# Kernel optimization log

Measured on AMD Instinct MI355X. Metric: run time of the kernel, lower is better.

Reference implementation:

```python
import jax, jax.numpy as jnp
import numpy as np

B, S, DIM, H, D = 4, 2048, 1024, 16, 64
WINDOW = 512  # max_mem_segments * window_size


def _rotary_angles(seq_len, dim_head):
    inv_freq = 1.0 / (10000.0 ** (jnp.arange(0, dim_head, 2, dtype=jnp.float32) / dim_head))
    freqs = jnp.arange(seq_len, dtype=jnp.float32)[:, None] * inv_freq[None, :]  # [S, D/2]
    return jnp.repeat(freqs, 2, axis=-1)  # [S, D] interleaved


def _rotate_half(x):
    x1 = x[..., 0::2]
    x2 = x[..., 1::2]
    return jnp.stack((-x2, x1), axis=-1).reshape(x.shape)


def _apply_rotary(x, angles):
    # x: [b h n d], angles: [n d]
    return x * jnp.cos(angles) + _rotate_half(x) * jnp.sin(angles)


def setup_inputs() -> dict:
    key = jax.random.key(0)
    ks = jax.random.split(key, 7)
    tokens = jax.random.normal(ks[0], (B, S, DIM), dtype=jnp.float32)
    value_residual = jax.random.normal(ks[1], (B, H, S, D), dtype=jnp.float32)
    s = 0.02
    Wq = jax.random.normal(ks[2], (DIM, H * D), dtype=jnp.float32) * s
    Wkv = jax.random.normal(ks[3], (DIM, 2 * H * D), dtype=jnp.float32) * s
    Wout = jax.random.normal(ks[4], (H * D, DIM), dtype=jnp.float32) * s
    Wgate = jax.random.normal(ks[5], (DIM, H), dtype=jnp.float32) * s
    Wmix = jax.random.normal(ks[6], (DIM, H), dtype=jnp.float32) * s
    return {"tokens": tokens, "value_residual": value_residual, "Wq": Wq,
            "Wkv": Wkv, "Wout": Wout, "Wgate": Wgate, "Wmix": Wmix}


def reference(tokens, value_residual, Wq, Wkv, Wout, Wgate, Wmix):
    b, n, dim = tokens.shape
    scale = D ** -0.5

    def split_heads(t):  # [b n (h d)] -> [b h n d]
        return t.reshape(b, n, H, D).transpose(0, 2, 1, 3)

    q = split_heads(tokens @ Wq)
    kv = tokens @ Wkv
    k = split_heads(kv[..., : H * D])
    v = split_heads(kv[..., H * D:])

    q = q * scale

    # value-residual lerp: v.lerp(value_residual, mix)
    mix = jax.nn.sigmoid(jnp.einsum('bnd,dh->bhn', tokens, Wmix))[..., None]  # [b h n 1]
    v = v + (value_residual - v) * mix

    angles = _rotary_angles(n, D)
    q = _apply_rotary(q, angles)
    k = _apply_rotary(k, angles)

    sim = jnp.einsum('bhid,bhjd->bhij', q, k)

    # fixed-window causal mask: dist = i - j; masked if dist < 0 or dist > WINDOW
    pos = jnp.arange(n)
    dist = pos[:, None] - pos[None, :]
    mask = (dist < 0) | (dist > WINDOW)
    neg = -jnp.finfo(sim.dtype).max
    sim = jnp.where(mask[None, None], neg, sim)

    attn = jax.nn.softmax(sim, axis=-1)
    out = jnp.einsum('bhij,bhjd->bhid', attn, v)

    gates = jax.nn.sigmoid(jnp.einsum('bnd,dh->bhn', tokens, Wgate))[..., None]  # [b h n 1]
    out = out * gates

    out = out.transpose(0, 2, 1, 3).reshape(b, n, H * D)
    return out @ Wout
```

## Files before the change

kernel.cpp:

```cpp
#include <hip/hip_runtime.h>

#define NH 16
#define SLEN 2048
#define DMODEL 1024
#define DHEAD 64
#define WIN 512
#define NB 4

typedef unsigned short u16;
typedef unsigned int u32;
typedef unsigned long long u64;
typedef __attribute__((ext_vector_type(8))) __bf16 bf16x8;
typedef __attribute__((ext_vector_type(4))) float floatx4;

__device__ __forceinline__ float b2f(u32 bits16) {
  union { u32 i; float f; } x; x.i = bits16 << 16; return x.f;
}
__device__ __forceinline__ u16 f2b(float f) {
  union { float f; u32 i; } x; x.f = f;
  u32 r = x.i + 0x7fffu + ((x.i >> 16) & 1u);
  return (u16)(r >> 16);
}

__device__ __forceinline__ void gl2lds16(const u16* g, u16* l) {
  __builtin_amdgcn_global_load_lds(
      (const __attribute__((address_space(1))) unsigned int*)g,
      (__attribute__((address_space(3))) unsigned int*)l, 16, 0, 0);
}

template<int OFF>
__device__ __forceinline__ bf16x8 ldsr128(u32 addr) {
  bf16x8 r;
  if constexpr (OFF == 0)
    asm volatile("ds_read_b128 %0, %1" : "=v"(r) : "v"(addr));
  else
    asm volatile("ds_read_b128 %0, %1 offset:%2" : "=v"(r) : "v"(addr), "i"(OFF));
  return r;
}

#define WAIT_VM6   asm volatile("s_waitcnt vmcnt(6)" ::: "memory")
#define WAIT_VM0   asm volatile("s_waitcnt vmcnt(0)" ::: "memory")
#define WAIT_LGKM8 asm volatile("s_waitcnt lgkmcnt(8)" ::: "memory")
#define WAIT_LGKM0 asm volatile("s_waitcnt lgkmcnt(0)" ::: "memory")
#define SCHEDB     __builtin_amdgcn_sched_barrier(0)

__global__ __launch_bounds__(256) void prep_all(
    const float* __restrict__ tokens, const float* __restrict__ Wq,
    const float* __restrict__ Wkv, const float* __restrict__ Wout,
    const float* __restrict__ Wmix, const float* __restrict__ Wgate,
    u64* __restrict__ tokA64, u16* __restrict__ WqkvT, u16* __restrict__ WoutT,
    u16* __restrict__ Wmg, float2* __restrict__ rtab) {
  __shared__ u16 T[64][72];
  const int blk = blockIdx.x, tid = threadIdx.x;
  if (blk < 8192) {
    int i = blk * 256 + tid;
    float4 f = reinterpret_cast<const float4*>(tokens)[i];
    union { u16 u[4]; u64 ll; } pk;
    pk.u[0] = f2b(f.x); pk.u[1] = f2b(f.y); pk.u[2] = f2b(f.z); pk.u[3] = f2b(f.w);
    tokA64[i] = pk.ll;
  } else if (blk < 9216) {
    const float* src; u16* dst; int ld, nb, n0, k0;
    if (blk < 8960) {
      int tile = blk - 8192;
      n0 = (tile % 48) * 64; k0 = (tile / 48) * 64;
      if (n0 < 1024) { src = Wq; ld = 1024; nb = n0; }
      else { src = Wkv; ld = 2048; nb = n0 - 1024; }
      dst = WqkvT;
    } else {
      int tile = blk - 8960;
      n0 = (tile % 16) * 64; k0 = (tile / 16) * 64;
      src = Wout; ld = 1024; nb = n0; dst = WoutT;
    }
#pragma unroll
    for (int i = 0; i < 16; ++i) {
      int e = i * 256 + tid;
      int kr = e >> 6, nc = e & 63;
      T[kr][nc] = f2b(src[(size_t)(k0 + kr) * ld + nb + nc]);
    }
    __syncthreads();
#pragma unroll
    for (int i = 0; i < 16; ++i) {
      int e = i * 256 + tid;
      int nr = e >> 6, kc = e & 63;
      dst[(size_t)(n0 + nr) * 1024 + k0 + kc] = T[kc][nr];
    }
  } else if (blk < 9344) {
    int idx = (blk - 9216) * 256 + tid;
    int n = idx >> 10, k = idx & 1023;
    float v = (n < 16) ? Wmix[k * 16 + n] : Wgate[k * 16 + (n - 16)];
    Wmg[idx] = f2b(v);
  } else {
    int idx = (blk - 9344) * 256 + tid;
    int s = idx >> 5, t = idx & 31;
    float inv = __expf((float)t * -0.2878231366f);
    float ang = (float)s * inv;
    float sn, cs;
    __sincosf(ang, &sn, &cs);
    rtab[idx] = make_float2(cs, sn);
  }
}

__global__ __launch_bounds__(128) void mixgate_mfma(const u16* __restrict__ A,
    const u16* __restrict__ Wmg, float* __restrict__ mixws, float* __restrict__ gatews) {
  const int lane = threadIdx.x & 63, w = threadIdx.x >> 6;
  const int lm = lane & 15, quad = lane >> 4;
  const int row0 = (blockIdx.x * 2 + w) * 16;

  floatx4 acc[2];
  acc[0] = (floatx4){0.f, 0.f, 0.f, 0.f};
  acc[1] = (floatx4){0.f, 0.f, 0.f, 0.f};

#pragma unroll 4
  for (int k0 = 0; k0 < 1024; k0 += 32) {
    bf16x8 af = *reinterpret_cast<const bf16x8*>(
        &A[(size_t)(row0 + lm) * 1024 + k0 + quad * 8]);
    bf16x8 bf[2];
#pragma unroll
    for (int nt = 0; nt < 2; ++nt)
      bf[nt] = *reinterpret_cast<const bf16x8*>(
          &Wmg[(size_t)(nt * 16 + lm) * 1024 + k0 + quad * 8]);
#pragma unroll
    for (int nt = 0; nt < 2; ++nt)
      acc[nt] = __builtin_amdgcn_mfma_f32_16x16x32_bf16(af, bf[nt], acc[nt], 0, 0, 0);
  }

#pragma unroll
  for (int r = 0; r < 4; ++r) {
    int grow = row0 + quad * 4 + r;
    int b = grow >> 11, s = grow & 2047;
#pragma unroll
    for (int nt = 0; nt < 2; ++nt) {
      int n = nt * 16 + lm;
      float sig = 1.0f / (1.0f + __expf(-acc[nt][r]));
      int h = n & 15;
      (n < 16 ? mixws : gatews)[(b * NH + h) * SLEN + s] = sig;
    }
  }
}

template<int MODE>
__global__ __launch_bounds__(512, 2) void gemm_pipe(
    const u16* __restrict__ A, const u16* __restrict__ Bt,
    float* __restrict__ C,
    u16* __restrict__ qws, u16* __restrict__ kws, u16* __restrict__ vws,
    const float* __restrict__ vres, const float* __restrict__ mixws,
    const float2* __restrict__ rtab, int N) {
  __shared__ u16 smem[73728];
  const int tid = threadIdx.x;
  const int nbx = N >> 7;
  const int wg = (blockIdx.x & 7) * (gridDim.x >> 3) + (blockIdx.x >> 3);
  const int bx = wg % nbx, by = wg / nbx;
  const int row0 = by * 256, col0 = bx * 128;
  const int w = tid >> 6, lane = tid & 63;
  const int wr = (w >> 1) * 64, wc = (w & 1) * 64;
  const int lm = lane & 15, quad = lane >> 4;
  const int NT = 16;
  const int sr = tid >> 3, sc = tid & 7;
  const int sl0 = (sr * 8 + sc) * 8;
  const u16* gA = A + (size_t)(row0 + sr) * 1024 + ((sc ^ (sr & 7)) << 3);
  const u16* gB = Bt + (size_t)(col0 + sr) * 1024 + ((sc ^ (sr & 7)) << 3);

  const u32 ldsbase = (u32)(size_t)(__attribute__((address_space(3))) u16*)smem;
  u32 arow[2], brow[2];
#pragma unroll
  for (int j = 0; j < 2; ++j) {
    u32 cslot = (u32)((j * 4 + quad) ^ (lm & 7));
    arow[j] = (u32)(wr + lm) * 128 + cslot * 16;
    brow[j] = (u32)(wc + lm) * 128 + cslot * 16;
  }

  floatx4 acc[4][4];
#pragma unroll
  for (int i = 0; i < 4; ++i)
#pragma unroll
    for (int j = 0; j < 4; ++j)
      acc[i][j] = (floatx4){0.f, 0.f, 0.f, 0.f};

  auto stage3 = [&](u16* Sa, u16* Sb, int ks, int half) {
    if (half == 0) {
      gl2lds16(gA + ks, Sa + sl0);
      gl2lds16(gA + 65536 + ks, Sa + 4096 + sl0);
      gl2lds16(gB + ks, Sb + sl0);
    } else {
      gl2lds16(gA + 131072 + ks, Sa + 8192 + sl0);
      gl2lds16(gA + 196608 + ks, Sa + 12288 + sl0);
      gl2lds16(gB + 65536 + ks, Sb + 4096 + sl0);
    }
  };

#pragma unroll
  for (int tt = 0; tt < 2; ++tt) {
    u16* Sa = smem + tt * 24576;
    u16* Sb = Sa + 16384;
    stage3(Sa, Sb, tt * 64, 0);
    stage3(Sa, Sb, tt * 64, 1);
  }

  int cur = 0;
  for (int t = 0; t < NT; ++t) {
    int sidx = cur + 2; if (sidx >= 3) sidx -= 3;
    u16* Sa = smem + sidx * 24576;
    u16* Sb = Sa + 16384;
    const int ks = (t + 2) << 6;
    const bool do_stage = t < NT - 2;
    const u32 abase = ldsbase + (u32)cur * 49152u;

    if (t < NT - 1) { WAIT_VM6; } else { WAIT_VM0; }
    __builtin_amdgcn_s_barrier();

    const u32 a0 = abase + arow[0], b0 = abase + 32768u + brow[0];
    const u32 a1 = abase + arow[1], b1 = abase + 32768u + brow[1];
    bf16x8 af0[4], bf0[4], af1[4], bf1[4];
    af0[0] = ldsr128<0>(a0);    af0[1] = ldsr128<2048>(a0);
    af0[2] = ldsr128<4096>(a0); af0[3] = ldsr128<6144>(a0);
    bf0[0] = ldsr128<0>(b0);    bf0[1] = ldsr128<2048>(b0);
    bf0[2] = ldsr128<4096>(b0); bf0[3] = ldsr128<6144>(b0);
    af1[0] = ldsr128<0>(a1);    af1[1] = ldsr128<2048>(a1);
    af1[2] = ldsr128<4096>(a1); af1[3] = ldsr128<6144>(a1);
    bf1[0] = ldsr128<0>(b1);    bf1[1] = ldsr128<2048>(b1);
    bf1[2] = ldsr128<4096>(b1); bf1[3] = ldsr128<6144>(b1);
    if (do_stage) { stage3(Sa, Sb, ks, 0); stage3(Sa, Sb, ks, 1); }
    SCHEDB;
    WAIT_LGKM8;
    SCHEDB;
    __builtin_amdgcn_s_setprio(1);
#pragma unroll
    for (int mt = 0; mt < 4; ++mt)
#pragma unroll
      for (int nt = 0; nt < 4; ++nt)
        acc[mt][nt] = __builtin_amdgcn_mfma_f32_16x16x32_bf16(
            af0[mt], bf0[nt], acc[mt][nt], 0, 0, 0);
    __builtin_amdgcn_s_setprio(0);
    WAIT_LGKM0;
    SCHEDB;
    __builtin_amdgcn_s_setprio(1);
#pragma unroll
    for (int mt = 0; mt < 4; ++mt)
#pragma unroll
      for (int nt = 0; nt < 4; ++nt)
        acc[mt][nt] = __builtin_amdgcn_mfma_f32_16x16x32_bf16(
            af1[mt], bf1[nt], acc[mt][nt], 0, 0, 0);
    __builtin_amdgcn_s_setprio(0);

    cur += 1; if (cur >= 3) cur -= 3;
  }

  if (MODE == 0) {
#pragma unroll
    for (int mt = 0; mt < 4; ++mt)
#pragma unroll
      for (int r = 0; r < 4; ++r) {
        int grow = row0 + wr + mt * 16 + quad * 4 + r;
#pragma unroll
        for (int nt = 0; nt < 4; ++nt)
          C[(size_t)grow * N + col0 + wc + nt * 16 + lm] = acc[mt][nt][r];
      }
  } else {
    const int seg = col0 >> 10;
    if (seg < 2) {
      u16* dst = seg ? kws : qws;
      const float qs = seg ? 1.0f : 0.125f;
      const int colb = (col0 & 1023) + wc;
#pragma unroll
      for (int mt = 0; mt < 4; ++mt)
#pragma unroll
        for (int r = 0; r < 4; ++r) {
          int sg = row0 + wr + mt * 16 + quad * 4 + r;
          int b = sg >> 11, s = sg & 2047;
#pragma unroll
          for (int nt = 0; nt < 4; ++nt) {
            int nn = colb + nt * 16 + lm;
            int h = nn >> 6, d = nn & 63;
            float val = acc[mt][nt][r] * qs;
            float2 cs = rtab[(s << 5) + (d >> 1)];
            float partner = __shfl_xor(val, 1);
            float o = (d & 1) ? fmaf(val, cs.x, partner * cs.y)
                              : fmaf(val, cs.x, -partner * cs.y);
            dst[((size_t)((b * NH + h) * SLEN + s)) * 64 + d] = f2b(o);
          }
        }
    } else {
      const int h0 = (col0 - 2048) >> 6;
      const int p = (w & 1);
      const int b = row0 >> 11, s0 = row0 & 2047;
      const int bh = b * NH + h0 + p;
      u16 (*Vt)[264] = reinterpret_cast<u16(*)[264]>(smem + p * 16896);
      __syncthreads();
#pragma unroll
      for (int mt = 0; mt < 4; ++mt)
#pragma unroll
        for (int nt = 0; nt < 4; ++nt) {
          const int d = nt * 16 + lm;
          const int sl = wr + mt * 16 + quad * 4;
          union { u16 u[4]; u64 ll; } pk;
#pragma unroll
          for (int r = 0; r < 4; ++r) {
            int s = s0 + sl + r;
            float val = acc[mt][nt][r];
            float mv = mixws[bh * SLEN + s];
            float o = val + (vres[((size_t)(bh * SLEN + s)) * 64 + d] - val) * mv;
            pk.u[r] = f2b(o);
          }
          *reinterpret_cast<u64*>(&Vt[d][sl]) = pk.ll;
        }
      __syncthreads();
#pragma unroll
      for (int it = 0; it < 8; ++it) {
        int idx = it * 512 + tid;
        int ph = idx >> 11, rem = idx & 2047;
        int d = rem >> 5, ch = rem & 31;
        const u16* src = smem + ph * 16896 + d * 264 + ch * 8;
        u16* dst = vws + ((size_t)((b * NH + h0 + ph) * 64 + d)) * SLEN + s0 + ch * 8;
        *reinterpret_cast<uint4*>(dst) = *reinterpret_cast<const uint4*>(src);
      }
    }
  }
}

__global__ __launch_bounds__(256) void attn_mfma_kernel(
    const u16* __restrict__ q, const u16* __restrict__ k, const u16* __restrict__ vt,
    const float* __restrict__ gate, u16* __restrict__ X) {
  __shared__ __align__(16) u16 Ks[2][4096];
  __shared__ __align__(16) u16 Vs[2][4096];
  __shared__ __align__(16) u16 Ps[4][16][72];
  const int tid = threadIdx.x;
  const int w = tid >> 6, lane = tid & 63;
  const int lm = lane & 15, quad = lane >> 4;
  const int sid = blockIdx.x;
  const int qt = (sid >> 3) & 31;
  const int bh = ((sid >> 8) << 3) | (sid & 7);
  const int h = bh & 15;
  const int b = bh >> 4;
  const int q0 = qt * 64;
  const size_t kqbase = (size_t)bh * SLEN * 64;
  const size_t vbase  = (size_t)bh * 64 * SLEN;

  bf16x8 qf[2];
  {
    const u16* qrow = q + kqbase + (size_t)(q0 + w * 16 + lm) * 64;
    qf[0] = *reinterpret_cast<const bf16x8*>(qrow + quad * 8);
    qf[1] = *reinterpret_cast<const bf16x8*>(qrow + 32 + quad * 8);
  }

  floatx4 o[4];
#pragma unroll
  for (int nt = 0; nt < 4; ++nt) o[nt] = (floatx4){0.f, 0.f, 0.f, 0.f};
  float lsum = 0.f;
  const int iq = q0 + w * 16 + lm;

  const int c_first = (q0 >= WIN) ? ((q0 - WIN) >> 6) : 0;
  const int c_last = q0 >> 6;

  const int sr = tid >> 3;
  const int scz = ((tid & 7) ^ (sr & 7)) * 8;
  const u32 ksbase = (u32)(size_t)(__attribute__((address_space(3))) u16*)&Ks[0][0];
  const u32 vsbase = (u32)(size_t)(__attribute__((address_space(3))) u16*)&Vs[0][0];
  const u32 psbase = (u32)(size_t)(__attribute__((address_space(3))) u16*)&Ps[0][0][0];
  const int rxa8 = lm & 7;
  const u32 rowoff = (u32)lm * 128 + (u32)((quad ^ rxa8) * 16);
  const u32 paddr = psbase + (u32)(w * 16 + lm) * 144 + (u32)quad * 16;

  auto stage = [&](int c, int buf) {
    const u16* kg = k + kqbase + (size_t)(c << 6) * 64;
    const u16* vg = vt + vbase + (c << 6);
    u16* Kd = &Ks[buf][0]; u16* Vd = &Vs[buf][0];
    gl2lds16(kg + sr * 64 + scz, Kd + tid * 8);
    gl2lds16(kg + (sr + 32) * 64 + scz, Kd + 2048 + tid * 8);
    gl2lds16(vg + (size_t)sr * SLEN + scz, Vd + tid * 8);
    gl2lds16(vg + (size_t)(sr + 32) * SLEN + scz, Vd + 2048 + tid * 8);
  };

  stage(c_first, 0);
  int cur = 0;
  for (int c = c_first; c <= c_last; ++c) {
    const int c0 = c << 6;
    __syncthreads();
    if (c < c_last) stage(c + 1, cur ^ 1);

    const u32 kof = ksbase + (u32)(cur << 13) + rowoff;
    const u32 kof4 = kof ^ 64u;
    bf16x8 k00 = ldsr128<0>(kof),     k01 = ldsr128<2048>(kof),
           k02 = ldsr128<4096>(kof),  k03 = ldsr128<6144>(kof);
    bf16x8 k10 = ldsr128<0>(kof4),    k11 = ldsr128<2048>(kof4),
           k12 = ldsr128<4096>(kof4), k13 = ldsr128<6144>(kof4);
    SCHEDB;
    WAIT_LGKM0;
    SCHEDB;
    floatx4 st[4];
    const floatx4 z4 = (floatx4){0.f, 0.f, 0.f, 0.f};
    __builtin_amdgcn_s_setprio(1);
    st[0] = __builtin_amdgcn_mfma_f32_16x16x32_bf16(k00, qf[0], z4, 0, 0, 0);
    st[0] = __builtin_amdgcn_mfma_f32_16x16x32_bf16(k10, qf[1], st[0], 0, 0, 0);
    st[1] = __builtin_amdgcn_mfma_f32_16x16x32_bf16(k01, qf[0], z4, 0, 0, 0);
    st[1] = __builtin_amdgcn_mfma_f32_16x16x32_bf16(k11, qf[1], st[1], 0, 0, 0);
    st[2] = __builtin_amdgcn_mfma_f32_16x16x32_bf16(k02, qf[0], z4, 0, 0, 0);
    st[2] = __builtin_amdgcn_mfma_f32_16x16x32_bf16(k12, qf[1], st[2], 0, 0, 0);
    st[3] = __builtin_amdgcn_mfma_f32_16x16x32_bf16(k03, qf[0], z4, 0, 0, 0);
    st[3] = __builtin_amdgcn_mfma_f32_16x16x32_bf16(k13, qf[1], st[3], 0, 0, 0);
    __builtin_amdgcn_s_setprio(0);

    const bool need_mask = (c == c_first && q0 >= WIN) || (c == c_last);
    if (need_mask) {
#pragma unroll
      for (int mt = 0; mt < 4; ++mt)
#pragma unroll
        for (int r = 0; r < 4; ++r) {
          int j = c0 + mt * 16 + quad * 4 + r;
          bool valid = (j <= iq) && (j >= iq - WIN);
          if (!valid) st[mt][r] = -3.0e38f;
        }
    }
    float p[4][4], psum = 0.f;
#pragma unroll
    for (int mt = 0; mt < 4; ++mt)
#pragma unroll
      for (int r = 0; r < 4; ++r) {
        p[mt][r] = __expf(st[mt][r]);
        psum += p[mt][r];
      }
    psum += __shfl_xor(psum, 16);
    psum += __shfl_xor(psum, 32);
    lsum += psum;
#pragma unroll
    for (int mt = 0; mt < 4; ++mt) {
      union { u16 u[4]; u64 ll; } pk;
#pragma unroll
      for (int r = 0; r < 4; ++r) pk.u[r] = f2b(p[mt][r]);
      *reinterpret_cast<u64*>(&Ps[w][lm][mt * 16 + quad * 4]) = pk.ll;
    }
    __builtin_amdgcn_wave_barrier();
    __builtin_amdgcn_s_waitcnt(0xC07F);
    __builtin_amdgcn_wave_barrier();

    bf16x8 pa0 = ldsr128<0>(paddr), pa1 = ldsr128<64>(paddr);
    const u32 vof = vsbase + (u32)(cur << 13) + rowoff;
    const u32 vof4 = vof ^ 64u;
    bf16x8 v00 = ldsr128<0>(vof),     v01 = ldsr128<2048>(vof),
           v02 = ldsr128<4096>(vof),  v03 = ldsr128<6144>(vof);
    bf16x8 v10 = ldsr128<0>(vof4),    v11 = ldsr128<2048>(vof4),
           v12 = ldsr128<4096>(vof4), v13 = ldsr128<6144>(vof4);
    SCHEDB;
    WAIT_LGKM0;
    SCHEDB;
    __builtin_amdgcn_s_setprio(1);
    o[0] = __builtin_amdgcn_mfma_f32_16x16x32_bf16(pa0, v00, o[0], 0, 0, 0);
    o[0] = __builtin_amdgcn_mfma_f32_16x16x32_bf16(pa1, v10, o[0], 0, 0, 0);
    o[1] = __builtin_amdgcn_mfma_f32_16x16x32_bf16(pa0, v01, o[1], 0, 0, 0);
    o[1] = __builtin_amdgcn_mfma_f32_16x16x32_bf16(pa1, v11, o[1], 0, 0, 0);
    o[2] = __builtin_amdgcn_mfma_f32_16x16x32_bf16(pa0, v02, o[2], 0, 0, 0);
    o[2] = __builtin_amdgcn_mfma_f32_16x16x32_bf16(pa1, v12, o[2], 0, 0, 0);
    o[3] = __builtin_amdgcn_mfma_f32_16x16x32_bf16(pa0, v03, o[3], 0, 0, 0);
    o[3] = __builtin_amdgcn_mfma_f32_16x16x32_bf16(pa1, v13, o[3], 0, 0, 0);
    __builtin_amdgcn_s_setprio(0);

    cur ^= 1;
  }
  float linv[4], g[4];
#pragma unroll
  for (int r = 0; r < 4; ++r) {
    linv[r] = 1.0f / __shfl(lsum, quad * 4 + r);
    g[r] = gate[bh * SLEN + q0 + w * 16 + quad * 4 + r];
  }
#pragma unroll
  for (int r = 0; r < 4; ++r) {
    int i = q0 + w * 16 + quad * 4 + r;
    u16* xrow = X + ((size_t)(b * SLEN + i)) * 1024 + h * 64;
#pragma unroll
    for (int nt = 0; nt < 4; ++nt)
      xrow[nt * 16 + lm] = f2b(o[nt][r] * linv[r] * g[r]);
  }
}

extern "C" void kernel_launch(void* const* d_in, const int* in_sizes, int n_in,
                              void* d_out, int out_size, void* d_ws, size_t ws_size,
                              hipStream_t stream) {
  (void)in_sizes; (void)n_in; (void)out_size; (void)ws_size;
  const float* tokens = (const float*)d_in[0];
  const float* vres   = (const float*)d_in[1];
  const float* Wq     = (const float*)d_in[2];
  const float* Wkv    = (const float*)d_in[3];
  const float* Wout   = (const float*)d_in[4];
  const float* Wgate  = (const float*)d_in[5];
  const float* Wmix   = (const float*)d_in[6];
  float* out = (float*)d_out;

  char* p = (char*)d_ws;
  auto alloc = [&](size_t bytes) { char* r = p; p += (bytes + 255) & ~(size_t)255; return r; };
  u16*  tokA   = (u16*)alloc(8192ull * 1024 * 2);
  u16*  WqkvT  = (u16*)alloc(3072ull * 1024 * 2);
  u16*  WoutT  = (u16*)alloc(1024ull * 1024 * 2);
  u16*  Wmg    = (u16*)alloc(32ull * 1024 * 2);
  float2* rtab = (float2*)alloc(65536ull * 8);
  u16*  qws    = (u16*)alloc(8388608ull * 2);
  u16*  kws    = (u16*)alloc(8388608ull * 2);
  u16*  vws    = (u16*)alloc(8388608ull * 2);
  u16*  Xws    = (u16*)alloc(8388608ull * 2);
  float* mixws = (float*)alloc(131072ull * 4);
  float* gatews= (float*)alloc(131072ull * 4);

  prep_all<<<9600, 256, 0, stream>>>(tokens, Wq, Wkv, Wout, Wmix, Wgate,
      (u64*)tokA, WqkvT, WoutT, Wmg, rtab);
  mixgate_mfma<<<256, 128, 0, stream>>>(tokA, Wmg, mixws, gatews);
  gemm_pipe<1><<<768, 512, 0, stream>>>(tokA, WqkvT, nullptr,
      qws, kws, vws, vres, mixws, rtab, 3072);
  attn_mfma_kernel<<<2048, 256, 0, stream>>>(qws, kws, vws, gatews, Xws);
  gemm_pipe<0><<<256, 512, 0, stream>>>(Xws, WoutT, out,
      nullptr, nullptr, nullptr, nullptr, nullptr, nullptr, 1024);
}
```

Before: 265.9 us.

## Shrink GEMM tiles to 128x128 with 256 threads and double-buffered LDS

Both projection GEMMs move from a 256x128 tile with 512 threads and a 3-stage LDS ring to a 128x128 tile with 256 threads and two LDS buffers. The next tile is prefetched right after a barrier rather than after issuing LDS reads, and the V-transpose epilogue is resized to match. This doubles the grid (1536 and 512 blocks) for better CU fill and lower LDS use per block. In exchange, each block reuses fewer operands and the pipeline is shallower, with an extra barrier per k-step.

After: 255.0 us. 4.1% less time.

```diff
diff --git a/kernel.cpp b/kernel.cpp
--- a/kernel.cpp
+++ b/kernel.cpp
@@ -38,7 +38,7 @@
   return r;
 }
 
-#define WAIT_VM6   asm volatile("s_waitcnt vmcnt(6)" ::: "memory")
+#define WAIT_VM8   asm volatile("s_waitcnt vmcnt(8)" ::: "memory")
 #define WAIT_VM0   asm volatile("s_waitcnt vmcnt(0)" ::: "memory")
 #define WAIT_LGKM8 asm volatile("s_waitcnt lgkmcnt(8)" ::: "memory")
 #define WAIT_LGKM0 asm volatile("s_waitcnt lgkmcnt(0)" ::: "memory")
@@ -139,18 +139,18 @@
 }
 
 template<int MODE>
-__global__ __launch_bounds__(512, 2) void gemm_pipe(
+__global__ __launch_bounds__(256, 2) void gemm_pipe(
     const u16* __restrict__ A, const u16* __restrict__ Bt,
     float* __restrict__ C,
     u16* __restrict__ qws, u16* __restrict__ kws, u16* __restrict__ vws,
     const float* __restrict__ vres, const float* __restrict__ mixws,
     const float2* __restrict__ rtab, int N) {
-  __shared__ u16 smem[73728];
+  __shared__ u16 smem[32768];
   const int tid = threadIdx.x;
   const int nbx = N >> 7;
   const int wg = (blockIdx.x & 7) * (gridDim.x >> 3) + (blockIdx.x >> 3);
   const int bx = wg % nbx, by = wg / nbx;
-  const int row0 = by * 256, col0 = bx * 128;
+  const int row0 = by * 128, col0 = bx * 128;
   const int w = tid >> 6, lane = tid & 63;
   const int wr = (w >> 1) * 64, wc = (w & 1) * 64;
   const int lm = lane & 15, quad = lane >> 4;
@@ -166,7 +166,7 @@
   for (int j = 0; j < 2; ++j) {
     u32 cslot = (u32)((j * 4 + quad) ^ (lm & 7));
     arow[j] = (u32)(wr + lm) * 128 + cslot * 16;
-    brow[j] = (u32)(wc + lm) * 128 + cslot * 16;
+    brow[j] = 16384u + (u32)(wc + lm) * 128 + cslot * 16;
   }
 
   floatx4 acc[4][4];
@@ -176,40 +176,33 @@
     for (int j = 0; j < 4; ++j)
       acc[i][j] = (floatx4){0.f, 0.f, 0.f, 0.f};
 
-  auto stage3 = [&](u16* Sa, u16* Sb, int ks, int half) {
-    if (half == 0) {
-      gl2lds16(gA + ks, Sa + sl0);
-      gl2lds16(gA + 65536 + ks, Sa + 4096 + sl0);
-      gl2lds16(gB + ks, Sb + sl0);
-    } else {
-      gl2lds16(gA + 131072 + ks, Sa + 8192 + sl0);
-      gl2lds16(gA + 196608 + ks, Sa + 12288 + sl0);
-      gl2lds16(gB + 65536 + ks, Sb + 4096 + sl0);
-    }
+  auto stage8 = [&](int buf, int t2) {
+    const int ks = t2 << 6;
+    u16* Sa = smem + buf * 16384;
+    u16* Sb = Sa + 8192;
+    gl2lds16(gA + ks, Sa + sl0);
+    gl2lds16(gA + 32 * 1024 + ks, Sa + 2048 + sl0);
+    gl2lds16(gA + 64 * 1024 + ks, Sa + 4096 + sl0);
+    gl2lds16(gA + 96 * 1024 + ks, Sa + 6144 + sl0);
+    gl2lds16(gB + ks, Sb + sl0);
+    gl2lds16(gB + 32 * 1024 + ks, Sb + 2048 + sl0);
+    gl2lds16(gB + 64 * 1024 + ks, Sb + 4096 + sl0);
+    gl2lds16(gB + 96 * 1024 + ks, Sb + 6144 + sl0);
   };
 
-#pragma unroll
-  for (int tt = 0; tt < 2; ++tt) {
-    u16* Sa = smem + tt * 24576;
-    u16* Sb = Sa + 16384;
-    stage3(Sa, Sb, tt * 64, 0);
-    stage3(Sa, Sb, tt * 64, 1);
-  }
-
-  int cur = 0;
+  stage8(0, 0);
   for (int t = 0; t < NT; ++t) {
-    int sidx = cur + 2; if (sidx >= 3) sidx -= 3;
-    u16* Sa = smem + sidx * 24576;
-    u16* Sb = Sa + 16384;
-    const int ks = (t + 2) << 6;
-    const bool do_stage = t < NT - 2;
-    const u32 abase = ldsbase + (u32)cur * 49152u;
-
-    if (t < NT - 1) { WAIT_VM6; } else { WAIT_VM0; }
+    const int cur = t & 1;
+    const u32 abase = ldsbase + (u32)cur * 32768u;
+
     __builtin_amdgcn_s_barrier();
-
-    const u32 a0 = abase + arow[0], b0 = abase + 32768u + brow[0];
-    const u32 a1 = abase + arow[1], b1 = abase + 32768u + brow[1];
+    if (t + 1 < NT) { stage8(cur ^ 1, t + 1); WAIT_VM8; }
+    else            { WAIT_VM0; }
+    __builtin_amdgcn_s_barrier();
+    SCHEDB;
+
+    const u32 a0 = abase + arow[0], b0 = abase + brow[0];
+    const u32 a1 = abase + arow[1], b1 = abase + brow[1];
     bf16x8 af0[4], bf0[4], af1[4], bf1[4];
     af0[0] = ldsr128<0>(a0);    af0[1] = ldsr128<2048>(a0);
     af0[2] = ldsr128<4096>(a0); af0[3] = ldsr128<6144>(a0);
@@ -219,7 +212,6 @@
     af1[2] = ldsr128<4096>(a1); af1[3] = ldsr128<6144>(a1);
     bf1[0] = ldsr128<0>(b1);    bf1[1] = ldsr128<2048>(b1);
     bf1[2] = ldsr128<4096>(b1); bf1[3] = ldsr128<6144>(b1);
-    if (do_stage) { stage3(Sa, Sb, ks, 0); stage3(Sa, Sb, ks, 1); }
     SCHEDB;
     WAIT_LGKM8;
     SCHEDB;
@@ -241,8 +233,6 @@
         acc[mt][nt] = __builtin_amdgcn_mfma_f32_16x16x32_bf16(
             af1[mt], bf1[nt], acc[mt][nt], 0, 0, 0);
     __builtin_amdgcn_s_setprio(0);
-
-    cur += 1; if (cur >= 3) cur -= 3;
   }
 
   if (MODE == 0) {
@@ -281,10 +271,10 @@
         }
     } else {
       const int h0 = (col0 - 2048) >> 6;
-      const int p = (w & 1);
+      const int p = w & 1;
       const int b = row0 >> 11, s0 = row0 & 2047;
       const int bh = b * NH + h0 + p;
-      u16 (*Vt)[264] = reinterpret_cast<u16(*)[264]>(smem + p * 16896);
+      u16* VtW = smem + p * 8704;
       __syncthreads();
 #pragma unroll
       for (int mt = 0; mt < 4; ++mt)
@@ -301,17 +291,17 @@
             float o = val + (vres[((size_t)(bh * SLEN + s)) * 64 + d] - val) * mv;
             pk.u[r] = f2b(o);
           }
-          *reinterpret_cast<u64*>(&Vt[d][sl]) = pk.ll;
+          *reinterpret_cast<u64*>(&VtW[d * 136 + sl]) = pk.ll;
         }
       __syncthreads();
 #pragma unroll
       for (int it = 0; it < 8; ++it) {
-        int idx = it * 512 + tid;
-        int ph = idx >> 11, rem = idx & 2047;
-        int d = rem >> 5, ch = rem & 31;
-        const u16* src = smem + ph * 16896 + d * 264 + ch * 8;
-        u16* dst = vws + ((size_t)((b * NH + h0 + ph) * 64 + d)) * SLEN + s0 + ch * 8;
-        *reinterpret_cast<uint4*>(dst) = *reinterpret_cast<const uint4*>(src);
+        int idx = it * 256 + tid;
+        int ph = idx >> 10, rem = idx & 1023;
+        int d = rem >> 4, ch = rem & 15;
+        const u16* src = smem + ph * 8704 + d * 136 + ch * 8;
+        u16* dstp = vws + ((size_t)((b * NH + h0 + ph) * 64 + d)) * SLEN + s0 + ch * 8;
+        *reinterpret_cast<uint4*>(dstp) = *reinterpret_cast<const uint4*>(src);
       }
     }
   }
@@ -501,9 +491,9 @@
   prep_all<<<9600, 256, 0, stream>>>(tokens, Wq, Wkv, Wout, Wmix, Wgate,
       (u64*)tokA, WqkvT, WoutT, Wmg, rtab);
   mixgate_mfma<<<256, 128, 0, stream>>>(tokA, Wmg, mixws, gatews);
-  gemm_pipe<1><<<768, 512, 0, stream>>>(tokA, WqkvT, nullptr,
+  gemm_pipe<1><<<1536, 256, 0, stream>>>(tokA, WqkvT, nullptr,
       qws, kws, vws, vres, mixws, rtab, 3072);
   attn_mfma_kernel<<<2048, 256, 0, stream>>>(qws, kws, vws, gatews, Xws);
-  gemm_pipe<0><<<256, 512, 0, stream>>>(Xws, WoutT, out,
+  gemm_pipe<0><<<512, 256, 0, stream>>>(Xws, WoutT, out,
       nullptr, nullptr, nullptr, nullptr, nullptr, nullptr, 1024);
 }
```
